# Performance work log

Hardware: AMD Instinct MI355X
Metric: run time of the kernel (lower is better)

## Reference

```python
import jax, jax.numpy as jnp
import numpy as np

N = 8192
IN_DIM, HID_DIM, OUT_DIM = 32, 64, 16


def setup_inputs() -> dict:
    key = jax.random.key(0)
    k1, k2, k3, k4, k5, k6, k7 = jax.random.split(key, 7)
    s1 = 1.0 / np.sqrt(IN_DIM)
    s2 = 1.0 / np.sqrt(HID_DIM)
    return {
        "adj1": jax.random.normal(k1, (N, N), jnp.float32),
        "adj2": jax.random.normal(k2, (N, N), jnp.float32),
        "features": jax.random.normal(k3, (N, IN_DIM), jnp.float32),
        # gc1 linear (shared across both aggregation branches)
        "W1": jax.random.uniform(k4, (IN_DIM, HID_DIM), jnp.float32, -s1, s1),
        "b1": jax.random.uniform(k5, (HID_DIM,), jnp.float32, -s1, s1),
        # gc2 linear
        "W2": jax.random.uniform(k6, (HID_DIM, OUT_DIM), jnp.float32, -s2, s2),
        "b2": jax.random.uniform(k7, (OUT_DIM,), jnp.float32, -s2, s2),
    }


def _gc_layer(adj1, adj2, x, W, b):
    # branch 1: aggregate -> shared linear -> relu
    o1 = jax.nn.relu(jnp.matmul(adj1, x) @ W + b)
    # branch 2: same linear weights
    o2 = jax.nn.relu(jnp.matmul(adj2, x) @ W + b)
    return o1 + o2


def reference(adj1, adj2, features, W1, b1, W2, b2):
    h1 = _gc_layer(adj1, adj2, features, W1, b1)  # [N, HID_DIM]
    h2 = _gc_layer(adj1, adj2, h1, W2, b2)        # [N, OUT_DIM]
    return h2
```

## Files before the change

### kernel.cpp

```cpp
#include <hip/hip_runtime.h>
#include <stdint.h>

#define NN 8192
#define IN_DIM 32
#define HID_DIM 64
#define OUT_DIM 16

typedef __attribute__((ext_vector_type(8))) short short8;
typedef __attribute__((ext_vector_type(4))) float f32x4;

__device__ __forceinline__ short f2bf_bits(float x){
  uint32_t u = __builtin_bit_cast(uint32_t, x);
  u += 0x7FFFu + ((u >> 16) & 1u);
  return (short)(u >> 16);
}

__device__ __forceinline__ short8 cvt8(f32x4 lo, f32x4 hi){
  short8 r;
  r[0]=f2bf_bits(lo[0]); r[1]=f2bf_bits(lo[1]); r[2]=f2bf_bits(lo[2]); r[3]=f2bf_bits(lo[3]);
  r[4]=f2bf_bits(hi[0]); r[5]=f2bf_bits(hi[1]); r[6]=f2bf_bits(hi[2]); r[7]=f2bf_bits(hi[3]);
  return r;
}

__global__ __launch_bounds__(256) void k_g(const float* __restrict__ X, const float* __restrict__ W1,
                                           short* __restrict__ Gt){
  const int b    = blockIdx.x;
  const int rb   = (b & 127) * 64;
  const int cg   = b >> 7;
  const int lane = threadIdx.x & 63;
  const int c    = cg * 4 + (threadIdx.x >> 6);
  const int r    = rb + lane;
  const float* xr = X + (size_t)r * IN_DIM;
  float acc = 0.f;
  #pragma unroll
  for (int k = 0; k < IN_DIM; ++k)
    acc += xr[k] * W1[(size_t)k * HID_DIM + c];
  Gt[(size_t)c * NN + r] = f2bf_bits(acc);
}

template<int REV>
__global__ __launch_bounds__(64, 2) void mm64(const float* __restrict__ adj1, const float* __restrict__ adj2,
                                              const short* __restrict__ Bt,
                                              float* __restrict__ P1, float* __restrict__ P2, int klen){
  __shared__ __align__(16) float sA[2][64 * 64];
  const int l     = threadIdx.x;
  const int strip = REV ? ((int)gridDim.x - 1 - (int)blockIdx.x) : (int)blockIdx.x;
  const int ks    = REV ? ((int)gridDim.y - 1 - (int)blockIdx.y) : (int)blockIdx.y;
  const int z     = REV ? (1 - (int)blockIdx.z) : (int)blockIdx.z;
  const float* __restrict__ adj = z ? adj2 : adj1;
  const int k0    = ks * klen;
  const int ngrp  = klen >> 6;
  const int phase = (strip + (z << 3)) & (ngrp - 1);
  const int rl    = l & 15;
  const int qh    = l >> 4;
  const size_t rowb = (size_t)strip * 64 * NN;

  auto gmap = [&](int t){
    const int tg = REV ? (phase + ngrp - 1 - t) : (phase + t);
    return tg & (ngrp - 1);
  };

  auto stage = [&](int t){
    if (t >= ngrp) return;
    const int g   = gmap(t);
    const int buf = t & 1;
    const size_t colb = (size_t)(k0 + g * 64);
    #pragma unroll
    for (int p = 0; p < 16; ++p){
      const int row = p * 4 + qh;
      const int sg  = rl ^ (row & 15);
      const float* s = adj + rowb + (size_t)row * NN + colb + sg * 4;
      __builtin_amdgcn_global_load_lds(
          (const __attribute__((address_space(1))) void*)s,
          (__attribute__((address_space(3))) void*)&sA[buf][p * 256 + l * 4], 16, 0, 0);
    }
  };

  auto loadB = [&](int t, short8 (&d)[2][4]){
    if (t >= ngrp) return;
    const int g = gmap(t);
    const size_t bk = (size_t)(k0 + g * 64) + qh * 8;
    #pragma unroll
    for (int j = 0; j < 2; ++j)
      #pragma unroll
      for (int f = 0; f < 4; ++f)
        d[j][f] = *(const short8*)(Bt + (size_t)(f * 16 + rl) * NN + bk + j * 32);
  };

  f32x4 acc[4][4];
  #pragma unroll
  for (int mi = 0; mi < 4; ++mi)
    #pragma unroll
    for (int f = 0; f < 4; ++f)
      acc[mi][f] = f32x4{0.f,0.f,0.f,0.f};

  auto compute = [&](int t, const short8 (&b)[2][4]){
    const float* sa = &sA[t & 1][0];
    #pragma unroll
    for (int j = 0; j < 2; ++j){
      const int g0 = j * 8 + qh * 2;
      #pragma unroll
      for (int mi = 0; mi < 4; ++mi){
        const int r = mi * 16 + rl;
        f32x4 lo = *(const f32x4*)(sa + r * 64 + (((g0    ) ^ rl) << 2));
        f32x4 hi = *(const f32x4*)(sa + r * 64 + (((g0 + 1) ^ rl) << 2));
        short8 fa = cvt8(lo, hi);
        #pragma unroll
        for (int f = 0; f < 4; ++f)
          acc[mi][f] = __builtin_amdgcn_mfma_f32_16x16x32_bf16(fa, b[j][f], acc[mi][f], 0, 0, 0);
      }
    }
  };

  short8 bA[2][4], bB[2][4];

  loadB(0, bA);
  stage(0);

  #pragma unroll 1
  for (int t = 0; t < ngrp; t += 2){
    loadB(t + 1, bB);
    stage(t + 1);
    asm volatile("s_waitcnt vmcnt(24)" ::: "memory");
    __builtin_amdgcn_sched_barrier(0);
    compute(t, bA);
    loadB(t + 2, bA);
    stage(t + 2);
    asm volatile("s_waitcnt vmcnt(24)" ::: "memory");
    __builtin_amdgcn_sched_barrier(0);
    compute(t + 1, bB);
  }

  float* P = z ? P2 : P1;
  #pragma unroll
  for (int mi = 0; mi < 4; ++mi){
    const int orow = strip * 64 + mi * 16 + qh * 4;
    float* p = P + ((size_t)ks * NN + orow) * HID_DIM + rl;
    #pragma unroll
    for (int r = 0; r < 4; ++r){
      #pragma unroll
      for (int f = 0; f < 4; ++f)
        p[(size_t)r * HID_DIM + f * 16] = acc[mi][f][r];
    }
  }
}

__global__ __launch_bounds__(256) void l1_combine(const float* __restrict__ Y1p, const float* __restrict__ Y2p,
                                                  const float* __restrict__ b1,
                                                  short* __restrict__ H1t, int S){
  __shared__ float sH[64][65];
  const int tid = threadIdx.x, lane = tid & 63, wave = tid >> 6;
  const int rb = blockIdx.x * 64;
  const float bc = b1[lane];
  #pragma unroll 4
  for (int rq = 0; rq < 16; ++rq){
    const int r = rq * 4 + wave;
    const int row = rb + r;
    float s1 = 0.f, s2 = 0.f;
    for (int sp = 0; sp < S; ++sp){
      s1 += Y1p[((size_t)sp * NN + row) * HID_DIM + lane];
      s2 += Y2p[((size_t)sp * NN + row) * HID_DIM + lane];
    }
    sH[r][lane] = fmaxf(s1 + bc, 0.f) + fmaxf(s2 + bc, 0.f);
  }
  __syncthreads();
  #pragma unroll 4
  for (int i = 0; i < 16; ++i){
    const int c = wave * 16 + i;
    H1t[(size_t)c * NN + rb + lane] = f2bf_bits(sH[lane][c]);
  }
}

__global__ __launch_bounds__(256) void l2_combine(const float* __restrict__ Z1p, const float* __restrict__ Z2p,
                                                  const float* __restrict__ W2, const float* __restrict__ b2,
                                                  float* __restrict__ out, int S){
  __shared__ float sW[HID_DIM * OUT_DIM];
  __shared__ float sb[OUT_DIM];
  __shared__ float sz[4][2][HID_DIM];
  const int tid = threadIdx.x;
  for (int i = tid; i < HID_DIM * OUT_DIM; i += 256) sW[i] = W2[i];
  if (tid < OUT_DIM) sb[tid] = b2[tid];
  const int sub = tid >> 6, t = tid & 63;
  const int row = blockIdx.x * 4 + sub;
  float s1 = 0.f, s2 = 0.f;
  for (int sp = 0; sp < S; ++sp){
    s1 += Z1p[((size_t)sp * NN + row) * HID_DIM + t];
    s2 += Z2p[((size_t)sp * NN + row) * HID_DIM + t];
  }
  sz[sub][0][t] = s1;
  sz[sub][1][t] = s2;
  __syncthreads();
  if (t < OUT_DIM){
    float a = sb[t], b = sb[t];
    #pragma unroll
    for (int k = 0; k < HID_DIM; ++k){
      a += sz[sub][0][k] * sW[k * OUT_DIM + t];
      b += sz[sub][1][k] * sW[k * OUT_DIM + t];
    }
    out[(size_t)row * OUT_DIM + t] = fmaxf(a, 0.f) + fmaxf(b, 0.f);
  }
}

extern "C" void kernel_launch(void* const* d_in, const int* in_sizes, int n_in,
                              void* d_out, int out_size, void* d_ws, size_t ws_size,
                              hipStream_t stream){
  const float* adj1 = (const float*)d_in[0];
  const float* adj2 = (const float*)d_in[1];
  const float* X    = (const float*)d_in[2];
  const float* W1   = (const float*)d_in[3];
  const float* b1   = (const float*)d_in[4];
  const float* W2   = (const float*)d_in[5];
  const float* b2   = (const float*)d_in[6];
  float* out = (float*)d_out;

  char* ws = (char*)d_ws;
  short* Gt  = (short*)ws;
  short* H1t = (short*)(ws + (size_t)1024 * 1024);
  const size_t off = (size_t)2 * 1024 * 1024;

  int S = 8;
  while (S > 1 && off + (size_t)S * 4 * 1024 * 1024 > ws_size) S >>= 1;
  float* P1 = (float*)(ws + off);
  float* P2 = P1 + (size_t)S * NN * HID_DIM;
  const int klen = NN / S;

  k_g        <<<dim3(2048),          dim3(256), 0, stream>>>(X, W1, Gt);
  mm64<0>    <<<dim3(NN / 64, S, 2), dim3(64),  0, stream>>>(adj1, adj2, Gt, P1, P2, klen);
  l1_combine <<<dim3(NN / 64),       dim3(256), 0, stream>>>(P1, P2, b1, H1t, S);
  mm64<1>    <<<dim3(NN / 64, S, 2), dim3(64),  0, stream>>>(adj1, adj2, H1t, P1, P2, klen);
  l2_combine <<<dim3(NN / 4),        dim3(256), 0, stream>>>(P1, P2, W2, b2, out, S);
}
```

Measured before the change: 269.2 us.

## Stage adjacency tiles through registers instead of direct global-to-LDS loads

The main GEMM kernel no longer issues global_load_lds directly into shared memory. It now loads adjacency tiles into registers and writes them to a swizzled LDS buffer one step later, with the K step shrunk from 64 to 32 columns. The pipeline is rewritten with explicit vmcnt waits, a separate epilogue, and half-size LDS buffers. This aims to hide global latency better and lower LDS pressure. In exchange it costs extra VGPRs, adds LDS write instructions, and doubles the loop iterations. There are also no barriers between the LDS writes and reads within the single wave.

```diff
diff --git a/kernel.cpp b/kernel.cpp
--- a/kernel.cpp
+++ b/kernel.cpp
@@ -39,20 +39,22 @@
 }
 
 template<int REV>
-__global__ __launch_bounds__(64, 2) void mm64(const float* __restrict__ adj1, const float* __restrict__ adj2,
-                                              const short* __restrict__ Bt,
-                                              float* __restrict__ P1, float* __restrict__ P2, int klen){
-  __shared__ __align__(16) float sA[2][64 * 64];
+__global__ __launch_bounds__(64, 2) void mm64r(const float* __restrict__ adj1, const float* __restrict__ adj2,
+                                               const short* __restrict__ Bt,
+                                               float* __restrict__ P1, float* __restrict__ P2, int klen){
+  __shared__ __align__(16) float sA[2][64 * 32];
   const int l     = threadIdx.x;
   const int strip = REV ? ((int)gridDim.x - 1 - (int)blockIdx.x) : (int)blockIdx.x;
   const int ks    = REV ? ((int)gridDim.y - 1 - (int)blockIdx.y) : (int)blockIdx.y;
   const int z     = REV ? (1 - (int)blockIdx.z) : (int)blockIdx.z;
   const float* __restrict__ adj = z ? adj2 : adj1;
   const int k0    = ks * klen;
-  const int ngrp  = klen >> 6;
+  const int ngrp  = klen >> 5;
   const int phase = (strip + (z << 3)) & (ngrp - 1);
   const int rl    = l & 15;
   const int qh    = l >> 4;
+  const int sr8   = l >> 3;
+  const int sg    = (l & 7) ^ sr8;
   const size_t rowb = (size_t)strip * 64 * NN;
 
   auto gmap = [&](int t){
@@ -60,31 +62,27 @@
     return tg & (ngrp - 1);
   };
 
-  auto stage = [&](int t){
-    if (t >= ngrp) return;
-    const int g   = gmap(t);
-    const int buf = t & 1;
-    const size_t colb = (size_t)(k0 + g * 64);
-    #pragma unroll
-    for (int p = 0; p < 16; ++p){
-      const int row = p * 4 + qh;
-      const int sg  = rl ^ (row & 15);
-      const float* s = adj + rowb + (size_t)row * NN + colb + sg * 4;
-      __builtin_amdgcn_global_load_lds(
-          (const __attribute__((address_space(1))) void*)s,
-          (__attribute__((address_space(3))) void*)&sA[buf][p * 256 + l * 4], 16, 0, 0);
-    }
-  };
-
-  auto loadB = [&](int t, short8 (&d)[2][4]){
-    if (t >= ngrp) return;
+  auto SL = [&](int t, f32x4 (&R)[8]){
     const int g = gmap(t);
-    const size_t bk = (size_t)(k0 + g * 64) + qh * 8;
-    #pragma unroll
-    for (int j = 0; j < 2; ++j)
-      #pragma unroll
-      for (int f = 0; f < 4; ++f)
-        d[j][f] = *(const short8*)(Bt + (size_t)(f * 16 + rl) * NN + bk + j * 32);
+    const float* base = adj + rowb + (size_t)(k0 + g * 32) + sg * 4;
+    #pragma unroll
+    for (int p = 0; p < 8; ++p)
+      R[p] = *(const f32x4*)(base + (size_t)(p * 8 + sr8) * NN);
+  };
+
+  auto DW = [&](const f32x4 (&R)[8], float* buf){
+    float* dst = buf + (l & 7) * 4;
+    #pragma unroll
+    for (int p = 0; p < 8; ++p)
+      *(f32x4*)(dst + (p * 8 + sr8) * 32) = R[p];
+  };
+
+  auto BL = [&](int t, short8 (&d)[4]){
+    const int g = gmap(t);
+    const size_t bk = (size_t)(k0 + g * 32) + qh * 8;
+    #pragma unroll
+    for (int f = 0; f < 4; ++f)
+      d[f] = *(const short8*)(Bt + (size_t)(f * 16 + rl) * NN + bk);
   };
 
   f32x4 acc[4][4];
@@ -94,42 +92,57 @@
     for (int f = 0; f < 4; ++f)
       acc[mi][f] = f32x4{0.f,0.f,0.f,0.f};
 
-  auto compute = [&](int t, const short8 (&b)[2][4]){
-    const float* sa = &sA[t & 1][0];
-    #pragma unroll
-    for (int j = 0; j < 2; ++j){
-      const int g0 = j * 8 + qh * 2;
+  auto compute = [&](const float* sa, const short8 (&b)[4]){
+    #pragma unroll
+    for (int mi = 0; mi < 4; ++mi){
+      const int row = mi * 16 + rl;
+      f32x4 lo = *(const f32x4*)(sa + row * 32 + (((qh * 2    ) ^ (rl & 7)) << 2));
+      f32x4 hi = *(const f32x4*)(sa + row * 32 + (((qh * 2 + 1) ^ (rl & 7)) << 2));
+      short8 fa = cvt8(lo, hi);
       #pragma unroll
-      for (int mi = 0; mi < 4; ++mi){
-        const int r = mi * 16 + rl;
-        f32x4 lo = *(const f32x4*)(sa + r * 64 + (((g0    ) ^ rl) << 2));
-        f32x4 hi = *(const f32x4*)(sa + r * 64 + (((g0 + 1) ^ rl) << 2));
-        short8 fa = cvt8(lo, hi);
-        #pragma unroll
-        for (int f = 0; f < 4; ++f)
-          acc[mi][f] = __builtin_amdgcn_mfma_f32_16x16x32_bf16(fa, b[j][f], acc[mi][f], 0, 0, 0);
-      }
-    }
-  };
-
-  short8 bA[2][4], bB[2][4];
-
-  loadB(0, bA);
-  stage(0);
+      for (int f = 0; f < 4; ++f)
+        acc[mi][f] = __builtin_amdgcn_mfma_f32_16x16x32_bf16(fa, b[f], acc[mi][f], 0, 0, 0);
+    }
+  };
+
+  f32x4 SA[8];
+  short8 bA[4], bB[4];
+
+  SL(0, SA); BL(0, bA);
 
   #pragma unroll 1
-  for (int t = 0; t < ngrp; t += 2){
-    loadB(t + 1, bB);
-    stage(t + 1);
-    asm volatile("s_waitcnt vmcnt(24)" ::: "memory");
-    __builtin_amdgcn_sched_barrier(0);
-    compute(t, bA);
-    loadB(t + 2, bA);
-    stage(t + 2);
-    asm volatile("s_waitcnt vmcnt(24)" ::: "memory");
-    __builtin_amdgcn_sched_barrier(0);
-    compute(t + 1, bB);
-  }
+  for (int t = 0; t < ngrp - 2; t += 2){
+    asm volatile("s_waitcnt vmcnt(4)" ::: "memory");
+    __builtin_amdgcn_sched_barrier(0);
+    DW(SA, &sA[0][0]);
+    SL(t + 1, SA);
+    asm volatile("s_waitcnt vmcnt(8)" ::: "memory");
+    __builtin_amdgcn_sched_barrier(0);
+    BL(t + 1, bB);
+    compute(&sA[0][0], bA);
+    asm volatile("s_waitcnt vmcnt(4)" ::: "memory");
+    __builtin_amdgcn_sched_barrier(0);
+    DW(SA, &sA[1][0]);
+    SL(t + 2, SA);
+    asm volatile("s_waitcnt vmcnt(8)" ::: "memory");
+    __builtin_amdgcn_sched_barrier(0);
+    BL(t + 2, bA);
+    compute(&sA[1][0], bB);
+  }
+  asm volatile("s_waitcnt vmcnt(4)" ::: "memory");
+  __builtin_amdgcn_sched_barrier(0);
+  DW(SA, &sA[0][0]);
+  SL(ngrp - 1, SA);
+  asm volatile("s_waitcnt vmcnt(8)" ::: "memory");
+  __builtin_amdgcn_sched_barrier(0);
+  BL(ngrp - 1, bB);
+  compute(&sA[0][0], bA);
+  asm volatile("s_waitcnt vmcnt(4)" ::: "memory");
+  __builtin_amdgcn_sched_barrier(0);
+  DW(SA, &sA[1][0]);
+  asm volatile("s_waitcnt vmcnt(0)" ::: "memory");
+  __builtin_amdgcn_sched_barrier(0);
+  compute(&sA[1][0], bB);
 
   float* P = z ? P2 : P1;
   #pragma unroll
@@ -225,8 +238,8 @@
   const int klen = NN / S;
 
   k_g        <<<dim3(2048),          dim3(256), 0, stream>>>(X, W1, Gt);
-  mm64<0>    <<<dim3(NN / 64, S, 2), dim3(64),  0, stream>>>(adj1, adj2, Gt, P1, P2, klen);
+  mm64r<0>   <<<dim3(NN / 64, S, 2), dim3(64),  0, stream>>>(adj1, adj2, Gt, P1, P2, klen);
   l1_combine <<<dim3(NN / 64),       dim3(256), 0, stream>>>(P1, P2, b1, H1t, S);
-  mm64<1>    <<<dim3(NN / 64, S, 2), dim3(64),  0, stream>>>(adj1, adj2, H1t, P1, P2, klen);
+  mm64r<1>   <<<dim3(NN / 64, S, 2), dim3(64),  0, stream>>>(adj1, adj2, H1t, P1, P2, klen);
   l2_combine <<<dim3(NN / 4),        dim3(256), 0, stream>>>(P1, P2, W2, b2, out, S);
 }
```

Result: faster. 262.0 us (-2.7%).

## Reshape adjacency tile to 32 rows by 128 columns with deeper prefetch

Applied to the files above, without the earlier changes.

Changes the per-wave adjacency tile from 64x64 to 32x128 floats and swizzles the LDS layout to match. This doubles the number of row-strip blocks so more waves are resident, and doubles the K depth handled per stage. The loop now prefetches two stages ahead, with a tail that drains them. The B-operand register footprint doubles, and each loaded B fragment is reused across only half as many rows, so B traffic per adj byte rises.

```diff
diff --git a/kernel.cpp b/kernel.cpp
--- a/kernel.cpp
+++ b/kernel.cpp
@@ -39,71 +39,71 @@
 }
 
 template<int REV>
-__global__ __launch_bounds__(64, 2) void mm64(const float* __restrict__ adj1, const float* __restrict__ adj2,
+__global__ __launch_bounds__(64, 2) void mm32(const float* __restrict__ adj1, const float* __restrict__ adj2,
                                               const short* __restrict__ Bt,
                                               float* __restrict__ P1, float* __restrict__ P2, int klen){
-  __shared__ __align__(16) float sA[2][64 * 64];
+  __shared__ __align__(16) float sA[2][32 * 128];
   const int l     = threadIdx.x;
   const int strip = REV ? ((int)gridDim.x - 1 - (int)blockIdx.x) : (int)blockIdx.x;
   const int ks    = REV ? ((int)gridDim.y - 1 - (int)blockIdx.y) : (int)blockIdx.y;
   const int z     = REV ? (1 - (int)blockIdx.z) : (int)blockIdx.z;
   const float* __restrict__ adj = z ? adj2 : adj1;
   const int k0    = ks * klen;
-  const int ngrp  = klen >> 6;
-  const int phase = (strip + (z << 3)) & (ngrp - 1);
+  const int ngrp  = klen >> 7;
+  const int phase = (strip + (z << 2)) & (ngrp - 1);
   const int rl    = l & 15;
   const int qh    = l >> 4;
-  const size_t rowb = (size_t)strip * 64 * NN;
+  const int shi   = l >> 5;
+  const int sgr   = l & 31;
+  const size_t rowb = (size_t)strip * 32 * NN;
 
   auto gmap = [&](int t){
     const int tg = REV ? (phase + ngrp - 1 - t) : (phase + t);
     return tg & (ngrp - 1);
   };
 
-  auto stage = [&](int t){
-    if (t >= ngrp) return;
-    const int g   = gmap(t);
-    const int buf = t & 1;
-    const size_t colb = (size_t)(k0 + g * 64);
+  auto SL = [&](int t, int buf){
+    const int g = gmap(t);
+    const size_t colb = (size_t)(k0 + g * 128);
     #pragma unroll
     for (int p = 0; p < 16; ++p){
-      const int row = p * 4 + qh;
-      const int sg  = rl ^ (row & 15);
-      const float* s = adj + rowb + (size_t)row * NN + colb + sg * 4;
+      const int row = p * 2 + shi;
+      const int gs  = sgr ^ (row & 7);
+      const float* s = adj + rowb + (size_t)row * NN + colb + gs * 4;
       __builtin_amdgcn_global_load_lds(
           (const __attribute__((address_space(1))) void*)s,
           (__attribute__((address_space(3))) void*)&sA[buf][p * 256 + l * 4], 16, 0, 0);
     }
   };
 
-  auto loadB = [&](int t, short8 (&d)[2][4]){
-    if (t >= ngrp) return;
+  auto BL = [&](int t, short8 (&d)[4][4]){
     const int g = gmap(t);
-    const size_t bk = (size_t)(k0 + g * 64) + qh * 8;
-    #pragma unroll
-    for (int j = 0; j < 2; ++j)
+    const size_t bk = (size_t)(k0 + g * 128) + qh * 8;
+    #pragma unroll
+    for (int j = 0; j < 4; ++j)
       #pragma unroll
       for (int f = 0; f < 4; ++f)
         d[j][f] = *(const short8*)(Bt + (size_t)(f * 16 + rl) * NN + bk + j * 32);
   };
 
-  f32x4 acc[4][4];
+  f32x4 acc[2][4];
   #pragma unroll
-  for (int mi = 0; mi < 4; ++mi)
+  for (int mi = 0; mi < 2; ++mi)
     #pragma unroll
     for (int f = 0; f < 4; ++f)
       acc[mi][f] = f32x4{0.f,0.f,0.f,0.f};
 
-  auto compute = [&](int t, const short8 (&b)[2][4]){
-    const float* sa = &sA[t & 1][0];
-    #pragma unroll
-    for (int j = 0; j < 2; ++j){
+  auto compute = [&](int buf, const short8 (&b)[4][4]){
+    const float* sa = &sA[buf][0];
+    #pragma unroll
+    for (int j = 0; j < 4; ++j){
       const int g0 = j * 8 + qh * 2;
       #pragma unroll
-      for (int mi = 0; mi < 4; ++mi){
-        const int r = mi * 16 + rl;
-        f32x4 lo = *(const f32x4*)(sa + r * 64 + (((g0    ) ^ rl) << 2));
-        f32x4 hi = *(const f32x4*)(sa + r * 64 + (((g0 + 1) ^ rl) << 2));
+      for (int mi = 0; mi < 2; ++mi){
+        const int r    = mi * 16 + rl;
+        const int base = (r >> 1) * 256 + (r & 1) * 128;
+        f32x4 lo = *(const f32x4*)(sa + base + (((g0    ) ^ (r & 7)) << 2));
+        f32x4 hi = *(const f32x4*)(sa + base + (((g0 + 1) ^ (r & 7)) << 2));
         short8 fa = cvt8(lo, hi);
         #pragma unroll
         for (int f = 0; f < 4; ++f)
@@ -112,29 +112,33 @@
     }
   };
 
-  short8 bA[2][4], bB[2][4];
-
-  loadB(0, bA);
-  stage(0);
+  short8 bA[4][4], bB[4][4];
+
+  BL(0, bA); SL(0, 0);
+  BL(1, bB); SL(1, 1);
 
   #pragma unroll 1
-  for (int t = 0; t < ngrp; t += 2){
-    loadB(t + 1, bB);
-    stage(t + 1);
-    asm volatile("s_waitcnt vmcnt(24)" ::: "memory");
+  for (int t = 0; t < ngrp - 2; t += 2){
+    asm volatile("s_waitcnt vmcnt(32)" ::: "memory");
     __builtin_amdgcn_sched_barrier(0);
-    compute(t, bA);
-    loadB(t + 2, bA);
-    stage(t + 2);
-    asm volatile("s_waitcnt vmcnt(24)" ::: "memory");
+    compute(0, bA);
+    BL(t + 2, bA); SL(t + 2, 0);
+    asm volatile("s_waitcnt vmcnt(32)" ::: "memory");
     __builtin_amdgcn_sched_barrier(0);
-    compute(t + 1, bB);
-  }
+    compute(1, bB);
+    BL(t + 3, bB); SL(t + 3, 1);
+  }
+  asm volatile("s_waitcnt vmcnt(32)" ::: "memory");
+  __builtin_amdgcn_sched_barrier(0);
+  compute(0, bA);
+  asm volatile("s_waitcnt vmcnt(0)" ::: "memory");
+  __builtin_amdgcn_sched_barrier(0);
+  compute(1, bB);
 
   float* P = z ? P2 : P1;
   #pragma unroll
-  for (int mi = 0; mi < 4; ++mi){
-    const int orow = strip * 64 + mi * 16 + qh * 4;
+  for (int mi = 0; mi < 2; ++mi){
+    const int orow = strip * 32 + mi * 16 + qh * 4;
     float* p = P + ((size_t)ks * NN + orow) * HID_DIM + rl;
     #pragma unroll
     for (int r = 0; r < 4; ++r){
@@ -213,20 +217,21 @@
   const float* b2   = (const float*)d_in[6];
   float* out = (float*)d_out;
 
+  const size_t MB = 1024 * 1024;
   char* ws = (char*)d_ws;
   short* Gt  = (short*)ws;
-  short* H1t = (short*)(ws + (size_t)1024 * 1024);
-  const size_t off = (size_t)2 * 1024 * 1024;
+  short* H1t = (short*)(ws + 1 * MB);
+  const size_t off = 2 * MB;
 
   int S = 8;
-  while (S > 1 && off + (size_t)S * 4 * 1024 * 1024 > ws_size) S >>= 1;
+  while (S > 1 && off + (size_t)S * 4 * MB > ws_size) S >>= 1;
   float* P1 = (float*)(ws + off);
   float* P2 = P1 + (size_t)S * NN * HID_DIM;
   const int klen = NN / S;
 
   k_g        <<<dim3(2048),          dim3(256), 0, stream>>>(X, W1, Gt);
-  mm64<0>    <<<dim3(NN / 64, S, 2), dim3(64),  0, stream>>>(adj1, adj2, Gt, P1, P2, klen);
+  mm32<0>    <<<dim3(NN / 32, S, 2), dim3(64),  0, stream>>>(adj1, adj2, Gt, P1, P2, klen);
   l1_combine <<<dim3(NN / 64),       dim3(256), 0, stream>>>(P1, P2, b1, H1t, S);
-  mm64<1>    <<<dim3(NN / 64, S, 2), dim3(64),  0, stream>>>(adj1, adj2, H1t, P1, P2, klen);
+  mm32<1>    <<<dim3(NN / 32, S, 2), dim3(64),  0, stream>>>(adj1, adj2, H1t, P1, P2, klen);
   l2_combine <<<dim3(NN / 4),        dim3(256), 0, stream>>>(P1, P2, W2, b2, out, S);
 }
```

New measurement: 294.2 us. 1.09x slower.
